# Optimization experiments

Hardware: AMD Instinct MI355X
Metric: run time of the kernel (lower is better)

The kernel has to match this reference:

```python
import jax, jax.numpy as jnp
import numpy as np
import math

H = 1024
N2 = 32  # N // 2 complex modes
L_LEN = 4096
LOG_DT_MIN = math.log(0.001)
LOG_DT_MAX = math.log(0.1)


def setup_inputs() -> dict:
    key = jax.random.key(0)
    k1, k2 = jax.random.split(key, 2)
    # log_dt ~ Uniform(log dt_min, log dt_max)
    log_dt = jax.random.uniform(k1, (H,), dtype=jnp.float32) * (LOG_DT_MAX - LOG_DT_MIN) + LOG_DT_MIN
    # C stored as real view of complex (H, N2): last dim = (real, imag)
    C = jax.random.normal(k2, (H, N2, 2), dtype=jnp.float32)
    log_A_real = jnp.log(0.5 * jnp.ones((H, N2), dtype=jnp.float32))
    A_imag = (math.pi * jnp.arange(N2, dtype=jnp.float32))[None, :] * jnp.ones((H, 1), jnp.float32)
    return {"log_dt": log_dt, "C": C, "log_A_real": log_A_real, "A_imag": A_imag, "L": L_LEN}


def reference(log_dt, C, log_A_real, A_imag, L):
    # dt: (H,)
    dt = jnp.exp(log_dt)
    # complex C: (H, N2)
    Cc = C[..., 0] + 1j * C[..., 1]
    # A = -exp(log_A_real) + i*A_imag : (H, N2)
    A = -jnp.exp(log_A_real) + 1j * A_imag
    dtA = A * dt[:, None]  # (H, N2)
    # discretized coefficient: C * (exp(dtA)-1)/A  (ZOH-like)
    Ck = Cc * (jnp.exp(dtA) - 1.0) / A  # (H, N2)
    # Vandermonde: exp(dtA * l) for l in [0, L)  -> (H, N2, L)
    V = jnp.exp(dtA[..., None] * jnp.arange(L, dtype=jnp.float32))
    # K = 2 * Re( sum_n Ck[h,n] * V[h,n,l] )  -> (H, L)
    K = 2.0 * jnp.einsum('hn,hnl->hl', Ck, V).real
    return K
```

## Files before the change

kernel.cpp:

```cpp
#include <hip/hip_runtime.h>
#include <math.h>


#define N2 32
#define L_LEN 4096
#define NTHREADS 256
#define PQS4 17

typedef float v2 __attribute__((ext_vector_type(2)));

__device__ __forceinline__ v2 vfma(v2 a, v2 b, v2 c) {
  return __builtin_elementwise_fma(a, b, c);
}

__global__ __launch_bounds__(NTHREADS, 4) void s4d_fused_kernel(
    const float* __restrict__ log_dt,
    const float* __restrict__ Cri,
    const float* __restrict__ log_A_real,
    const float* __restrict__ A_imag,
    float* __restrict__ out)
{
  const int h = blockIdx.x;
  const int t = threadIdx.x;
  const int a = t >> 4;
  const int b = t & 15;

  __shared__ float2 s_w[N2], s_w16[N2], s_ck[N2];
  __shared__ float4 s_Wri[N2 / 2];
  __shared__ float4 s_Wpq[N2 / 2];
  __shared__ float4 s_P[16 * PQS4];
  __shared__ float4 s_Q[16 * PQS4];

  if (t < N2) {
    const int n = t;
    const int idx = h * N2 + n;
    const double dt = exp((double)log_dt[h]);
    const double Ar = -exp((double)log_A_real[idx]);
    const double Ai = (double)A_imag[idx];
    const double xr = dt * Ar;
    const double xi = dt * Ai;
    const double ex = exp(xr);
    const double wr = ex * cos(xi);
    const double wi = ex * sin(xi);
    const double nr = wr - 1.0, ni = wi;
    const double inv = 1.0 / (Ar * Ar + Ai * Ai);
    const double fr = (nr * Ar + ni * Ai) * inv;
    const double fi = (ni * Ar - nr * Ai) * inv;
    const double c0 = (double)Cri[idx * 2 + 0];
    const double c1 = (double)Cri[idx * 2 + 1];
    s_ck[n] = make_float2((float)(2.0 * (c0 * fr - c1 * fi)),
                          (float)(2.0 * (c0 * fi + c1 * fr)));
    s_w[n] = make_float2((float)wr, (float)wi);
    double ar = wr, ai2 = wi;
#pragma unroll
    for (int k = 0; k < 4; ++k) {
      const double tr = ar * ar - ai2 * ai2;
      const double ti = 2.0 * ar * ai2;
      ar = tr; ai2 = ti;
    }
    s_w16[n] = make_float2((float)ar, (float)ai2);
#pragma unroll
    for (int k = 0; k < 4; ++k) {
      const double tr = ar * ar - ai2 * ai2;
      const double ti = 2.0 * ar * ai2;
      ar = tr; ai2 = ti;
    }
    float* Wri_f = (float*)s_Wri;
    float* Wpq_f = (float*)s_Wpq;
    const int pbase = (n >> 1) * 4 + (n & 1);
    Wri_f[pbase + 0] = (float)ar;
    Wri_f[pbase + 2] = (float)ai2;
    Wpq_f[pbase + 0] = (float)(2.0 * ar);
    Wpq_f[pbase + 2] = (float)(-(ar * ar + ai2 * ai2));
  }
  __syncthreads();

  if (t < 64) {
    const int n = t & 31;
    const int comp = n & 1;
    const int np = n >> 1;
    if (t < 32) {
      float* Pf = (float*)s_P;
      const float2 g = s_w16[n];
      float pr = 1.0f, pi = 0.0f;
#pragma unroll
      for (int aa = 0; aa < 16; ++aa) {
        const int base = (aa * PQS4 + np) * 4 + comp;
        Pf[base + 0] = pr;
        Pf[base + 2] = pi;
        const float tr = fmaf(pr, g.x, -(pi * g.y));
        const float ti = fmaf(pr, g.y, pi * g.x);
        pr = tr; pi = ti;
      }
    } else {
      float* Qf = (float*)s_Q;
      const float2 w = s_w[n];
      const float2 c = s_ck[n];
      float qr = c.x, qi = c.y;
#pragma unroll
      for (int bb = 0; bb < 16; ++bb) {
        const int base = (bb * PQS4 + np) * 4 + comp;
        Qf[base + 0] = qr;
        Qf[base + 2] = qi;
        const float tr = fmaf(qr, w.x, -(qi * w.y));
        const float ti = fmaf(qr, w.y, qi * w.x);
        qr = tr; qi = ti;
      }
    }
  }
  __syncthreads();

  v2 acc[16];
#pragma unroll
  for (int j = 0; j < 16; ++j) acc[j] = (v2){0.0f, 0.0f};

  const float4* Pa = s_P + a * PQS4;
  const float4* Qb = s_Q + b * PQS4;

#pragma unroll
  for (int np = 0; np < N2 / 2; ++np) {
    const float4 P4 = Pa[np];
    const float4 Q4 = Qb[np];
    const float4 Wri4 = s_Wri[np];
    const float4 Wpq4 = s_Wpq[np];
    const v2 Prp = (v2){P4.x, P4.y}, Pip = (v2){P4.z, P4.w};
    const v2 Qrp = (v2){Q4.x, Q4.y}, Qip = (v2){Q4.z, Q4.w};
    const v2 Wrp = (v2){Wri4.x, Wri4.y}, Wip = (v2){Wri4.z, Wri4.w};
    const v2 pp  = (v2){Wpq4.x, Wpq4.y}, mqp = (v2){Wpq4.z, Wpq4.w};

    const v2 Brp = vfma(Prp, Qrp, -(Pip * Qip));
    const v2 Bip = vfma(Prp, Qip, Pip * Qrp);
    v2 s0 = Brp;
    v2 s1 = vfma(Brp, Wrp, -(Bip * Wip));
    acc[0] += s0;
    acc[1] += s1;
#pragma unroll
    for (int j = 2; j < 16; ++j) {
      const v2 s2 = vfma(pp, s1, mqp * s0);
      acc[j] += s2;
      s0 = s1; s1 = s2;
    }
  }

  float* o = out + (size_t)h * L_LEN + t;
#pragma unroll
  for (int j = 0; j < 16; ++j) o[j * NTHREADS] = acc[j].x + acc[j].y;
}

extern "C" void kernel_launch(void* const* d_in, const int* in_sizes, int n_in,
                              void* d_out, int out_size, void* d_ws, size_t ws_size,
                              hipStream_t stream) {
  const float* log_dt     = (const float*)d_in[0];
  const float* Cri        = (const float*)d_in[1];
  const float* log_A_real = (const float*)d_in[2];
  const float* A_imag     = (const float*)d_in[3];
  float* out = (float*)d_out;
  const int H = in_sizes[0];

  s4d_fused_kernel<<<dim3(H), dim3(NTHREADS), 0, stream>>>(
      log_dt, Cri, log_A_real, A_imag, out);
}
```

Before: 74.88 us.

## Split S4D into parallel prep kernel and two-block-per-channel sweep kernel

Moves the per-mode double-precision coefficient setup into a separate fully parallel prep kernel that writes powers of w into a workspace. The sweep kernel then runs two blocks per channel, each covering half of L by starting P at w^2048, which halves the per-thread accumulator count and allows higher occupancy. The cost is an extra kernel launch and a round trip through global workspace, plus a fallback to the old fused kernel when the workspace is too small.

```diff
diff --git a/kernel.cpp b/kernel.cpp
--- a/kernel.cpp
+++ b/kernel.cpp
@@ -6,11 +6,177 @@
 #define L_LEN 4096
 #define NTHREADS 256
 #define PQS4 17
+#define NJ 8
 
 typedef float v2 __attribute__((ext_vector_type(2)));
 
 __device__ __forceinline__ v2 vfma(v2 a, v2 b, v2 c) {
   return __builtin_elementwise_fma(a, b, c);
+}
+
+__global__ __launch_bounds__(256) void s4d_prep(
+    const float* __restrict__ log_dt,
+    const float* __restrict__ Cri,
+    const float* __restrict__ log_A_real,
+    const float* __restrict__ A_imag,
+    float4* __restrict__ ws0,
+    float4* __restrict__ ws1,
+    float4* __restrict__ ws2,
+    int total)
+{
+  const int i = blockIdx.x * 256 + threadIdx.x;
+  if (i >= total) return;
+  const int h = i >> 5;
+  const double dt = exp((double)log_dt[h]);
+  const double Ar = -exp((double)log_A_real[i]);
+  const double Ai = (double)A_imag[i];
+  const double xr = dt * Ar;
+  const double xi = dt * Ai;
+  const double ex = exp(xr);
+  const double wr = ex * cos(xi);
+  const double wi = ex * sin(xi);
+  const double nr = wr - 1.0, ni = wi;
+  const double inv = 1.0 / (Ar * Ar + Ai * Ai);
+  const double fr = (nr * Ar + ni * Ai) * inv;
+  const double fi = (ni * Ar - nr * Ai) * inv;
+  const double c0 = (double)Cri[i * 2 + 0];
+  const double c1 = (double)Cri[i * 2 + 1];
+  ws0[i] = make_float4((float)wr, (float)wi,
+                       (float)(2.0 * (c0 * fr - c1 * fi)),
+                       (float)(2.0 * (c0 * fi + c1 * fr)));
+  double ar = wr, ai2 = wi;
+#pragma unroll
+  for (int k = 0; k < 4; ++k) {
+    const double tr = ar * ar - ai2 * ai2;
+    const double ti = 2.0 * ar * ai2;
+    ar = tr; ai2 = ti;
+  }
+  const float w16r = (float)ar, w16i = (float)ai2;
+#pragma unroll
+  for (int k = 0; k < 4; ++k) {
+    const double tr = ar * ar - ai2 * ai2;
+    const double ti = 2.0 * ar * ai2;
+    ar = tr; ai2 = ti;
+  }
+  const double Wr = ar, Wi = ai2;
+#pragma unroll
+  for (int k = 0; k < 3; ++k) {
+    const double tr = ar * ar - ai2 * ai2;
+    const double ti = 2.0 * ar * ai2;
+    ar = tr; ai2 = ti;
+  }
+  ws1[i] = make_float4(w16r, w16i, (float)ar, (float)ai2);
+  ws2[i] = make_float4((float)Wr, (float)Wi,
+                       (float)(2.0 * Wr), (float)(-(Wr * Wr + Wi * Wi)));
+}
+
+__global__ __launch_bounds__(NTHREADS, 8) void s4d_sweep(
+    const float4* __restrict__ ws0,
+    const float4* __restrict__ ws1,
+    const float4* __restrict__ ws2,
+    float* __restrict__ out)
+{
+  const int bid = blockIdx.x;
+  const int h = bid >> 1;
+  const int s = bid & 1;
+  const int t = threadIdx.x;
+  const int a = t >> 4;
+  const int b = t & 15;
+
+  __shared__ float2 s_w[N2], s_ck[N2];
+  __shared__ float4 s_Wri[N2 / 2];
+  __shared__ float4 s_Wpq[N2 / 2];
+  __shared__ float4 s_P[16 * PQS4];
+  __shared__ float4 s_Q[16 * PQS4];
+
+  float4 f1 = make_float4(0.f, 0.f, 0.f, 0.f);
+  if (t < N2) {
+    const int n = t;
+    const float4 f0 = ws0[h * N2 + n];
+    f1 = ws1[h * N2 + n];
+    const float4 f2 = ws2[h * N2 + n];
+    s_w[n] = make_float2(f0.x, f0.y);
+    s_ck[n] = make_float2(f0.z, f0.w);
+    float* Wri_f = (float*)s_Wri;
+    float* Wpq_f = (float*)s_Wpq;
+    const int pbase = (n >> 1) * 4 + (n & 1);
+    Wri_f[pbase + 0] = f2.x;
+    Wri_f[pbase + 2] = f2.y;
+    Wpq_f[pbase + 0] = f2.z;
+    Wpq_f[pbase + 2] = f2.w;
+  }
+  if (t < 64) {
+    const int n = t & 31;
+    const int comp = n & 1;
+    const int np = n >> 1;
+    if (t < 32) {
+      float* Pf = (float*)s_P;
+      const float gx = f1.x, gy = f1.y;
+      float pr, pi;
+      if (s == 0) { pr = 1.0f; pi = 0.0f; }
+      else        { pr = f1.z; pi = f1.w; }
+#pragma unroll
+      for (int aa = 0; aa < 16; ++aa) {
+        const int base = (aa * PQS4 + np) * 4 + comp;
+        Pf[base + 0] = pr;
+        Pf[base + 2] = pi;
+        const float tr = fmaf(pr, gx, -(pi * gy));
+        const float ti = fmaf(pr, gy, pi * gx);
+        pr = tr; pi = ti;
+      }
+    } else {
+      float* Qf = (float*)s_Q;
+      const float2 w = s_w[n];
+      const float2 c = s_ck[n];
+      float qr = c.x, qi = c.y;
+#pragma unroll
+      for (int bb = 0; bb < 16; ++bb) {
+        const int base = (bb * PQS4 + np) * 4 + comp;
+        Qf[base + 0] = qr;
+        Qf[base + 2] = qi;
+        const float tr = fmaf(qr, w.x, -(qi * w.y));
+        const float ti = fmaf(qr, w.y, qi * w.x);
+        qr = tr; qi = ti;
+      }
+    }
+  }
+  __syncthreads();
+
+  v2 acc[NJ];
+#pragma unroll
+  for (int j = 0; j < NJ; ++j) acc[j] = (v2){0.0f, 0.0f};
+
+  const float4* Pa = s_P + a * PQS4;
+  const float4* Qb = s_Q + b * PQS4;
+
+#pragma unroll
+  for (int np = 0; np < N2 / 2; ++np) {
+    const float4 P4 = Pa[np];
+    const float4 Q4 = Qb[np];
+    const float4 Wri4 = s_Wri[np];
+    const float4 Wpq4 = s_Wpq[np];
+    const v2 Prp = (v2){P4.x, P4.y}, Pip = (v2){P4.z, P4.w};
+    const v2 Qrp = (v2){Q4.x, Q4.y}, Qip = (v2){Q4.z, Q4.w};
+    const v2 Wrp = (v2){Wri4.x, Wri4.y}, Wip = (v2){Wri4.z, Wri4.w};
+    const v2 pp  = (v2){Wpq4.x, Wpq4.y}, mqp = (v2){Wpq4.z, Wpq4.w};
+
+    const v2 Brp = vfma(Prp, Qrp, -(Pip * Qip));
+    const v2 Bip = vfma(Prp, Qip, Pip * Qrp);
+    v2 s0 = Brp;
+    v2 s1 = vfma(Brp, Wrp, -(Bip * Wip));
+    acc[0] += s0;
+    acc[1] += s1;
+#pragma unroll
+    for (int j = 2; j < NJ; ++j) {
+      const v2 s2 = vfma(pp, s1, mqp * s0);
+      acc[j] += s2;
+      s0 = s1; s1 = s2;
+    }
+  }
+
+  float* o = out + (size_t)h * L_LEN + s * (L_LEN / 2) + t;
+#pragma unroll
+  for (int j = 0; j < NJ; ++j) o[j * NTHREADS] = acc[j].x + acc[j].y;
 }
 
 __global__ __launch_bounds__(NTHREADS, 4) void s4d_fused_kernel(
@@ -156,7 +322,18 @@
   const float* A_imag     = (const float*)d_in[3];
   float* out = (float*)d_out;
   const int H = in_sizes[0];
-
-  s4d_fused_kernel<<<dim3(H), dim3(NTHREADS), 0, stream>>>(
-      log_dt, Cri, log_A_real, A_imag, out);
-}
+  const int total = H * N2;
+  const size_t need = (size_t)total * 3 * sizeof(float4);
+
+  if (d_ws != nullptr && ws_size >= need) {
+    float4* ws0 = (float4*)d_ws;
+    float4* ws1 = ws0 + total;
+    float4* ws2 = ws1 + total;
+    s4d_prep<<<dim3((total + 255) / 256), dim3(256), 0, stream>>>(
+        log_dt, Cri, log_A_real, A_imag, ws0, ws1, ws2, total);
+    s4d_sweep<<<dim3(H * 2), dim3(NTHREADS), 0, stream>>>(ws0, ws1, ws2, out);
+  } else {
+    s4d_fused_kernel<<<dim3(H), dim3(NTHREADS), 0, stream>>>(
+        log_dt, Cri, log_A_real, A_imag, out);
+  }
+}
```

Result: slower. 78.24 us (+4.5%).
